# Optimization experiments

Measured on AMD Instinct MI355X. Metric: run time of the kernel, lower is better.

The kernel has to match this reference:

```python
import jax, jax.numpy as jnp
import numpy as np

B, N, DEG, LOOKBACK, DIM, OUT = 256, 512, 16, 5, 64, 6
E = B * N * DEG            # 2,097,152 directed edges
NN = B * N                 # 131,072 nodes
K1 = int(np.ceil(0.8 * N))    # 410 nodes kept per graph after pool1
K2 = int(np.ceil(0.8 * K1))   # 328 nodes kept per graph after pool2


def setup_inputs():
    key = jax.random.key(0)
    ks = jax.random.split(key, 14)
    x = jax.random.normal(ks[0], (NN, LOOKBACK), jnp.float32)
    # per-graph random edges, then shift into the global node index space
    local = jax.random.randint(ks[1], (2, E), 0, N)
    offsets = jnp.repeat(jnp.arange(B, dtype=jnp.int32) * N, N * DEG)
    edge_index = local + offsets[None, :]

    def lin(k, fi, fo):
        return jax.random.normal(k, (fi, fo), jnp.float32) / np.sqrt(fi)

    return {
        "x": x,
        "edge_index": edge_index,
        "c1_Wl": lin(ks[2], LOOKBACK, DIM), "c1_bl": jnp.zeros((DIM,), jnp.float32),
        "c1_Wr": lin(ks[3], LOOKBACK, DIM),
        "pool1_w": jax.random.normal(ks[4], (DIM,), jnp.float32) / np.sqrt(DIM),
        "c2_Wl": lin(ks[5], DIM, DIM), "c2_bl": jnp.zeros((DIM,), jnp.float32),
        "c2_Wr": lin(ks[6], DIM, DIM),
        "pool2_w": jax.random.normal(ks[7], (DIM,), jnp.float32) / np.sqrt(DIM),
        "lin1_W": lin(ks[8], 2 * DIM, DIM), "lin1_b": jnp.zeros((DIM,), jnp.float32),
        "lin2_W": lin(ks[9], DIM, OUT), "lin2_b": jnp.zeros((OUT,), jnp.float32),
    }


def _sage(x, src, dst, valid, Wl, bl, Wr, n_nodes):
    # PyG SAGEConv: out = lin_l(mean_{j->i} x_j) + lin_r(x_i); empty nbhd -> 0
    msg = x[src] * valid[:, None]
    s = jax.ops.segment_sum(msg, dst, num_segments=n_nodes)
    deg = jax.ops.segment_sum(valid, dst, num_segments=n_nodes)
    mean = s / jnp.maximum(deg, 1.0)[:, None]
    return mean @ Wl + bl + x @ Wr


def _topk(x, w, nb, npg, k):
    # PyG TopKPooling: score = tanh(x.w/||w||), keep top-k per graph, scale kept rows
    score = jnp.tanh((x @ w) / jnp.linalg.norm(w))
    vals, idx = jax.lax.top_k(score.reshape(nb, npg), k)     # [nb, k]
    perm = (idx + (jnp.arange(nb) * npg)[:, None]).reshape(-1)
    return x[perm] * vals.reshape(-1, 1), perm


def _readout(x, nb, k):
    r = x.reshape(nb, k, -1)
    return jnp.concatenate([r.max(axis=1), r.mean(axis=1)], axis=1)  # [gmp | gap]


def reference(x, edge_index, c1_Wl, c1_bl, c1_Wr, pool1_w,
              c2_Wl, c2_bl, c2_Wr, pool2_w, lin1_W, lin1_b, lin2_W, lin2_b):
    src, dst = edge_index[0], edge_index[1]
    valid0 = jnp.ones((E,), jnp.float32)

    h = jax.nn.relu(_sage(x, src, dst, valid0, c1_Wl, c1_bl, c1_Wr, NN))
    h, perm1 = _topk(h, pool1_w, B, N, K1)
    x1 = _readout(h, B, K1)

    # filter_adj: remap edges to pooled node ids, mask dropped edges
    n1 = B * K1
    inv = jnp.full((NN,), -1, jnp.int32).at[perm1].set(jnp.arange(n1, dtype=jnp.int32))
    s1, d1 = inv[src], inv[dst]
    valid1 = ((s1 >= 0) & (d1 >= 0)).astype(jnp.float32)
    s1 = jnp.maximum(s1, 0)
    d1 = jnp.maximum(d1, 0)

    h = jax.nn.relu(_sage(h, s1, d1, valid1, c2_Wl, c2_bl, c2_Wr, n1))
    h, _ = _topk(h, pool2_w, B, K1, K2)
    x2 = _readout(h, B, K2)

    z = x1 + x2
    z = jax.nn.relu(z @ lin1_W + lin1_b)
    return z @ lin2_W + lin2_b
```

## Files before the change

### kernel.cpp

```cpp
#include <hip/hip_runtime.h>
#include <hip/hip_bf16.h>

#define BGR   256
#define NPG1  512
#define DEG   16
#define EPG   (NPG1 * DEG)
#define LB    5
#define DIM   64
#define OUTF  6
#define NN    (BGR * NPG1)
#define EDG   (BGR * EPG)
#define K1    410
#define K2    328
#define N1    (BGR * K1)
#define K1P   (K1 + 1)
#define NR    (BGR * K1P)
#define CSRW  48
#define CSRW1 56
#define GRIDW (NR / 64)
#define GRIDA (N1 / 16)

__global__ __launch_bounds__(512)
void s1_csr_score_kernel(const float* __restrict__ x,
                         const int* __restrict__ eidx,
                         const float* __restrict__ Wl,
                         const float* __restrict__ bl,
                         const float* __restrict__ Wr,
                         const float* __restrict__ pw,
                         float* __restrict__ meanv,
                         float* __restrict__ sc1g) {
    __shared__ __align__(16) float xl[NPG1 * LB];
    __shared__ unsigned short lcsr[CSRW1 * NPG1];
    __shared__ int lcnt[NPG1];

    const int g = blockIdx.x, t = threadIdx.x;
    const int* __restrict__ src = eidx;
    const int* __restrict__ dst = eidx + EDG;

    {
        const float4* x4 = (const float4*)(x + (size_t)g * (NPG1 * LB));
        float4* xl4 = (float4*)xl;
        #pragma unroll
        for (int k = 0; k < 2; ++k) {
            int i = k * 512 + t;
            if (i < NPG1 * LB / 4) xl4[i] = x4[i];
        }
        lcnt[t] = 0;
    }
    __syncthreads();

    const int ebase = g * EPG;
    for (int k = 0; k < EPG / 512; ++k) {
        int e = ebase + k * 512 + t;
        int s = src[e] & (NPG1 - 1);
        int d = dst[e] & (NPG1 - 1);
        int slot = atomicAdd(&lcnt[d], 1);
        if (slot < CSRW1) lcsr[slot * NPG1 + d] = (unsigned short)s;
    }
    __syncthreads();

    const int dgf = lcnt[t];
    const int dg  = min(dgf, CSRW1);
    float s0 = 0.f, s1 = 0.f, s2 = 0.f, s3 = 0.f, s4 = 0.f;
    for (int k = 0; k < dg; ++k) {
        int s = lcsr[k * NPG1 + t];
        const float* xp = xl + s * LB;
        s0 += xp[0]; s1 += xp[1]; s2 += xp[2]; s3 += xp[3]; s4 += xp[4];
    }
    const float invd = 1.f / fmaxf((float)dgf, 1.f);
    float m[LB]  = { s0 * invd, s1 * invd, s2 * invd, s3 * invd, s4 * invd };
    float xv[LB];
    const int n = g * NPG1 + t;
    #pragma unroll
    for (int j = 0; j < LB; ++j) { xv[j] = xl[t * LB + j]; meanv[(size_t)n * LB + j] = m[j]; }

    const float4* Wl4 = (const float4*)Wl;
    const float4* Wr4 = (const float4*)Wr;
    const float4* bl4 = (const float4*)bl;
    const float4* pw4 = (const float4*)pw;
    float p = 0.f, q = 0.f;
    #pragma unroll 4
    for (int d4 = 0; d4 < DIM / 4; ++d4) {
        float4 bb = bl4[d4];
        float4 ww = pw4[d4];
        float4 h = bb;
        #pragma unroll
        for (int j = 0; j < LB; ++j) {
            float4 a = Wl4[j * (DIM / 4) + d4];
            float4 b = Wr4[j * (DIM / 4) + d4];
            h.x += m[j] * a.x + xv[j] * b.x;
            h.y += m[j] * a.y + xv[j] * b.y;
            h.z += m[j] * a.z + xv[j] * b.z;
            h.w += m[j] * a.w + xv[j] * b.w;
        }
        h.x = fmaxf(h.x, 0.f); h.y = fmaxf(h.y, 0.f);
        h.z = fmaxf(h.z, 0.f); h.w = fmaxf(h.w, 0.f);
        p += h.x * ww.x + h.y * ww.y + h.z * ww.z + h.w * ww.w;
        q += ww.x * ww.x + ww.y * ww.y + ww.z * ww.z + ww.w * ww.w;
    }
    sc1g[n] = tanhf(p / sqrtf(q));
}

__global__ __launch_bounds__(512)
void s1_rankpool_csr2_kernel(const float* __restrict__ x,
                             const float* __restrict__ meanv,
                             const float* __restrict__ sc1g,
                             const int* __restrict__ eidx,
                             const float* __restrict__ Wl,
                             const float* __restrict__ bl,
                             const float* __restrict__ Wr,
                             float* __restrict__ h1p,
                             float* __restrict__ x1buf,
                             unsigned short* __restrict__ csr2,
                             int* __restrict__ indeg) {
    __shared__ __align__(16) float sc[NPG1];
    __shared__ int   rnk[NPG1];
    __shared__ float redmx[8 * DIM];
    __shared__ float redsm[8 * DIM];
    __shared__ __align__(16) unsigned short lcsr2[K1 * CSRW];
    __shared__ int   lcnt2[K1];

    const int g = blockIdx.x, t = threadIdx.x;
    const int wid = t >> 6, lane = t & 63;
    const int* __restrict__ src = eidx;
    const int* __restrict__ dst = eidx + EDG;

    sc[t] = sc1g[g * NPG1 + t];
    if (t < DIM) h1p[((size_t)g * K1P + K1) * DIM + t] = 0.f;
    if (t < K1) lcnt2[t] = 0;
    {
        const int fill = (K1 << 16) | K1;
        int* li = (int*)lcsr2;
        for (int i = t; i < K1 * CSRW / 2; i += 512) li[i] = fill;
    }
    __syncthreads();

    {
        float my = sc[t];
        int r = 0;
        const float4* sc4 = (const float4*)sc;
        #pragma unroll 4
        for (int j4 = 0; j4 < NPG1 / 4; ++j4) {
            float4 v = sc4[j4];
            int j = 4 * j4;
            r += (v.x > my) | ((v.x == my) & (j     < t));
            r += (v.y > my) | ((v.y == my) & (j + 1 < t));
            r += (v.z > my) | ((v.z == my) & (j + 2 < t));
            r += (v.w > my) | ((v.w == my) & (j + 3 < t));
        }
        rnk[t] = r;
    }
    __syncthreads();

    const int ebase = g * EPG;
    for (int k = 0; k < EPG / 512; ++k) {
        int e = ebase + k * 512 + t;
        int rs = rnk[src[e] & (NPG1 - 1)];
        int rd = rnk[dst[e] & (NPG1 - 1)];
        if (rs < K1 && rd < K1) {
            int slot = atomicAdd(&lcnt2[rd], 1);
            if (slot < CSRW) lcsr2[rd * CSRW + slot] = (unsigned short)rs;
        }
    }

    float wlv[LB], wrv[LB];
    #pragma unroll
    for (int j = 0; j < LB; ++j) { wlv[j] = Wl[j * DIM + lane]; wrv[j] = Wr[j * DIM + lane]; }
    const float blv = bl[lane];

    float mx = -INFINITY, sm = 0.f;
    for (int n = wid; n < NPG1; n += 8) {
        int r = rnk[n];
        if (r >= K1) continue;
        const float* mp = meanv + (size_t)(g * NPG1 + n) * LB;
        const float* xp = x + (size_t)(g * NPG1 + n) * LB;
        float al = 0.f, ar = 0.f;
        #pragma unroll
        for (int j = 0; j < LB; ++j) {
            al += mp[j] * wlv[j];
            ar += xp[j] * wrv[j];
        }
        float acc = fmaxf(blv + al + ar, 0.f);
        float v = acc * sc[n];
        h1p[((size_t)g * K1P + r) * DIM + lane] = v;
        mx = fmaxf(mx, v);
        sm += v;
    }
    redmx[wid * DIM + lane] = mx;
    redsm[wid * DIM + lane] = sm;
    __syncthreads();

    if (wid == 0) {
        float m2 = redmx[lane], s2 = redsm[lane];
        #pragma unroll
        for (int w = 1; w < 8; ++w) {
            m2 = fmaxf(m2, redmx[w * DIM + lane]);
            s2 += redsm[w * DIM + lane];
        }
        x1buf[g * 2 * DIM + lane]       = m2;
        x1buf[g * 2 * DIM + DIM + lane] = s2 * (1.0f / (float)K1);
    }

    {
        const int4* ls4 = (const int4*)lcsr2;
        int4* gs4 = (int4*)(csr2 + (size_t)g * K1 * CSRW);
        for (int i = t; i < K1 * CSRW / 8; i += 512) gs4[i] = ls4[i];
        if (t < K1) indeg[g * K1 + t] = min(lcnt2[t], CSRW);
    }
}

__global__ __launch_bounds__(512)
void gemm2_kernel(float* __restrict__ hY,
                  float* __restrict__ Yr,
                  const float* __restrict__ Wl,
                  const float* __restrict__ bl,
                  const float* __restrict__ Wr) {
    __shared__ __align__(16) float wls[DIM * DIM];
    __shared__ __align__(16) float wrs[DIM * DIM];
    __shared__ __align__(16) float rt[64 * DIM];

    const int t = threadIdx.x, wid = t >> 6, lane = t & 63;
    const int nb = (int)blockIdx.x * 64;

    {
        const float4* W4l = (const float4*)Wl;
        const float4* W4r = (const float4*)Wr;
        const float4* R4  = (const float4*)&hY[(size_t)nb * DIM];
        float4* a = (float4*)wls;
        float4* b = (float4*)wrs;
        float4* r = (float4*)rt;
        #pragma unroll
        for (int k = 0; k < 2; ++k) {
            a[k * 512 + t] = W4l[k * 512 + t];
            b[k * 512 + t] = W4r[k * 512 + t];
            r[k * 512 + t] = R4[k * 512 + t];
        }
    }
    __syncthreads();

    const int r0 = wid * 8;
    float accl[8] = {0.f,0.f,0.f,0.f,0.f,0.f,0.f,0.f};
    float accr[8] = {0.f,0.f,0.f,0.f,0.f,0.f,0.f,0.f};
    #pragma unroll 4
    for (int j4 = 0; j4 < DIM / 4; ++j4) {
        const int jb = 4 * j4 * DIM + lane;
        float w0 = wls[jb],           w1 = wls[jb + DIM];
        float w2 = wls[jb + 2 * DIM], w3 = wls[jb + 3 * DIM];
        float u0 = wrs[jb],           u1 = wrs[jb + DIM];
        float u2 = wrs[jb + 2 * DIM], u3 = wrs[jb + 3 * DIM];
        #pragma unroll
        for (int i = 0; i < 8; ++i) {
            float4 a = *(const float4*)&rt[(r0 + i) * DIM + 4 * j4];
            accl[i] += a.x * w0 + a.y * w1 + a.z * w2 + a.w * w3;
            accr[i] += a.x * u0 + a.y * u1 + a.z * u2 + a.w * u3;
        }
    }
    const float bv = bl[lane];
    #pragma unroll
    for (int i = 0; i < 8; ++i) {
        hY[(size_t)(nb + r0 + i) * DIM + lane] = accl[i];
        Yr[(size_t)(nb + r0 + i) * DIM + lane] = accr[i] + bv;
    }
}

__global__ __launch_bounds__(256)
void gather2_kernel(const float* __restrict__ Yl,
                    float* __restrict__ Yh,
                    const unsigned short* __restrict__ csr2,
                    const int* __restrict__ indeg,
                    const float* __restrict__ pw,
                    float* __restrict__ sc2g) {
    const int t = threadIdx.x, wid = t >> 6, lane = t & 63;
    const int cid = ((int)blockIdx.x & 7) * (GRIDA / 8) + ((int)blockIdx.x >> 3);
    const int nb = __builtin_amdgcn_readfirstlane(cid * 16 + wid * 4);

    const float pwv = pw[lane];
    float q = pwv * pwv;
    #pragma unroll
    for (int o = 32; o; o >>= 1) q += __shfl_xor(q, o);
    const float inv_nrm = 1.f / sqrtf(q);

    #pragma unroll
    for (int i = 0; i < 4; ++i) {
        const int n  = nb + i;
        const int dg = indeg[n];
        const int g  = n / K1;
        const int lr = n - g * K1;
        const float* __restrict__ bp = Yl + (size_t)g * K1P * DIM;
        const int4* cr = (const int4*)(csr2 + (size_t)n * CSRW);
        float a0 = 0.f, a1 = 0.f;
        const int it = (dg + 7) >> 3;
        for (int kc = 0; kc < it; ++kc) {
            int4 wv = cr[kc];
            a0 += bp[((wv.x & 0xffff) << 6) + lane];
            a1 += bp[((wv.x >> 16)    << 6) + lane];
            a0 += bp[((wv.y & 0xffff) << 6) + lane];
            a1 += bp[((wv.y >> 16)    << 6) + lane];
            a0 += bp[((wv.z & 0xffff) << 6) + lane];
            a1 += bp[((wv.z >> 16)    << 6) + lane];
            a0 += bp[((wv.w & 0xffff) << 6) + lane];
            a1 += bp[((wv.w >> 16)    << 6) + lane];
        }
        const float invd = 1.f / fmaxf((float)dg, 1.f);
        float* yrow = Yh + (size_t)(g * K1P + lr) * DIM;
        const float h = fmaxf((a0 + a1) * invd + yrow[lane], 0.f);
        yrow[lane] = h;
        float p = h * pwv;
        #pragma unroll
        for (int o = 32; o; o >>= 1) p += __shfl_xor(p, o);
        if (lane == 0) sc2g[n] = tanhf(p * inv_nrm);
    }
}

__global__ __launch_bounds__(512)
void pool2_mlp_kernel(const float* __restrict__ sc2g,
                      const float* __restrict__ h2,
                      const float* __restrict__ x1buf,
                      const float* __restrict__ W1,
                      const float* __restrict__ b1,
                      const float* __restrict__ W2,
                      const float* __restrict__ b2,
                      float* __restrict__ out) {
    __shared__ __align__(16) float sc2[412];
    __shared__ int   rnk2[K1];
    __shared__ float redmx[8 * DIM];
    __shared__ float redsm[8 * DIM];
    __shared__ float zy[2 * DIM + DIM];

    const int g = blockIdx.x, t = threadIdx.x;
    const int wid = t >> 6, lane = t & 63;

    if (t < K1) sc2[t] = sc2g[g * K1 + t];
    if (t >= K1 && t < 412) sc2[t] = -INFINITY;
    __syncthreads();

    if (t < K1) {
        float my = sc2[t];
        int r = 0;
        const float4* sc4 = (const float4*)sc2;
        #pragma unroll 4
        for (int j4 = 0; j4 < 103; ++j4) {
            float4 v = sc4[j4];
            int j = 4 * j4;
            r += (v.x > my) | ((v.x == my) & (j     < t));
            r += (v.y > my) | ((v.y == my) & (j + 1 < t));
            r += (v.z > my) | ((v.z == my) & (j + 2 < t));
            r += (v.w > my) | ((v.w == my) & (j + 3 < t));
        }
        rnk2[t] = r;
    }
    __syncthreads();

    float mx = -INFINITY, sm = 0.f;
    for (int n = wid; n < K1; n += 8) {
        if (rnk2[n] < K2) {
            float v = h2[((size_t)g * K1P + n) * DIM + lane] * sc2[n];
            mx = fmaxf(mx, v);
            sm += v;
        }
    }
    redmx[wid * DIM + lane] = mx;
    redsm[wid * DIM + lane] = sm;
    __syncthreads();
    if (wid == 0) {
        float m2 = redmx[lane], s2 = redsm[lane];
        #pragma unroll
        for (int w = 1; w < 8; ++w) {
            m2 = fmaxf(m2, redmx[w * DIM + lane]);
            s2 += redsm[w * DIM + lane];
        }
        zy[lane]       = x1buf[g * 2 * DIM + lane]       + m2;
        zy[DIM + lane] = x1buf[g * 2 * DIM + DIM + lane] + s2 * (1.0f / (float)K2);
    }
    __syncthreads();

    if (t < DIM) {
        float a = b1[t];
        #pragma unroll 8
        for (int j = 0; j < 2 * DIM; ++j) a += zy[j] * W1[j * DIM + t];
        zy[2 * DIM + t] = fmaxf(a, 0.f);
    }
    __syncthreads();
    if (t < OUTF) {
        float a = b2[t];
        #pragma unroll
        for (int j = 0; j < DIM; ++j) a += zy[2 * DIM + j] * W2[j * OUTF + t];
        out[g * OUTF + t] = a;
    }
}

extern "C" void kernel_launch(void* const* d_in, const int* in_sizes, int n_in,
                              void* d_out, int out_size, void* d_ws, size_t ws_size,
                              hipStream_t stream) {
    (void)in_sizes; (void)n_in; (void)out_size; (void)ws_size;
    const float* x       = (const float*)d_in[0];
    const int*   eidx    = (const int*)d_in[1];
    const float* c1_Wl   = (const float*)d_in[2];
    const float* c1_bl   = (const float*)d_in[3];
    const float* c1_Wr   = (const float*)d_in[4];
    const float* pool1_w = (const float*)d_in[5];
    const float* c2_Wl   = (const float*)d_in[6];
    const float* c2_bl   = (const float*)d_in[7];
    const float* c2_Wr   = (const float*)d_in[8];
    const float* pool2_w = (const float*)d_in[9];
    const float* lin1_W  = (const float*)d_in[10];
    const float* lin1_b  = (const float*)d_in[11];
    const float* lin2_W  = (const float*)d_in[12];
    const float* lin2_b  = (const float*)d_in[13];
    float* out = (float*)d_out;

    char* w = (char*)d_ws;
    size_t off = 0;
    auto alloc = [&](size_t bytes) {
        void* p = w + off;
        off = (off + bytes + 255) & ~(size_t)255;
        return p;
    };
    float* h1p   = (float*)alloc((size_t)NR * DIM * 4);
    float* x1buf = (float*)alloc((size_t)BGR * 2 * DIM * 4);
    float* sc2g  = (float*)alloc((size_t)N1 * 4);
    int*   indeg = (int*)  alloc((size_t)N1 * 4);
    float* Yh    = (float*)alloc((size_t)NR * DIM * 4);
    unsigned short* csr2 = (unsigned short*)alloc((size_t)N1 * CSRW * 2);
    float* meanv = (float*)alloc((size_t)NN * LB * 4);
    float* sc1g  = (float*)alloc((size_t)NN * 4);

    float* Yl = h1p;

    s1_csr_score_kernel<<<BGR, 512, 0, stream>>>(x, eidx, c1_Wl, c1_bl, c1_Wr,
                                                 pool1_w, meanv, sc1g);
    s1_rankpool_csr2_kernel<<<BGR, 512, 0, stream>>>(x, meanv, sc1g, eidx,
                                                     c1_Wl, c1_bl, c1_Wr,
                                                     h1p, x1buf, csr2, indeg);
    gemm2_kernel<<<GRIDW, 512, 0, stream>>>(h1p, Yh, c2_Wl, c2_bl, c2_Wr);
    gather2_kernel<<<GRIDA, 256, 0, stream>>>(Yl, Yh, csr2, indeg, pool2_w, sc2g);
    pool2_mlp_kernel<<<BGR, 512, 0, stream>>>(sc2g, Yh, x1buf, lin1_W, lin1_b,
                                              lin2_W, lin2_b, out);
}
```

Baseline: 178.0 us.

## Fuse stage-1 CSR/score and rank-pool kernels, build pooled CSR from LDS CSR

Merges the two per-graph stage-1 kernels into one block so mean aggregates, scores and x stay in shared memory instead of round-tripping through global meanv/sc1g buffers. The pooled-graph CSR is now built per destination node by filtering the stage-1 LDS CSR through the rank table, which replaces a second pass over global edge indices and its shared-memory atomics. The cost is a much larger shared-memory footprint per block, which lowers occupancy. The CSR neighbor order also becomes deterministic per thread rather than set by atomic order.

New measurement: 165.8 us. -6.8%, faster.

```diff
diff --git a/kernel.cpp b/kernel.cpp
--- a/kernel.cpp
+++ b/kernel.cpp
@@ -21,19 +21,29 @@
 #define GRIDA (N1 / 16)
 
 __global__ __launch_bounds__(512)
-void s1_csr_score_kernel(const float* __restrict__ x,
-                         const int* __restrict__ eidx,
-                         const float* __restrict__ Wl,
-                         const float* __restrict__ bl,
-                         const float* __restrict__ Wr,
-                         const float* __restrict__ pw,
-                         float* __restrict__ meanv,
-                         float* __restrict__ sc1g) {
+void s1_mega_kernel(const float* __restrict__ x,
+                    const int* __restrict__ eidx,
+                    const float* __restrict__ Wl,
+                    const float* __restrict__ bl,
+                    const float* __restrict__ Wr,
+                    const float* __restrict__ pw,
+                    float* __restrict__ h1p,
+                    float* __restrict__ x1buf,
+                    unsigned short* __restrict__ csr2,
+                    int* __restrict__ indeg) {
     __shared__ __align__(16) float xl[NPG1 * LB];
-    __shared__ unsigned short lcsr[CSRW1 * NPG1];
-    __shared__ int lcnt[NPG1];
+    __shared__ __align__(16) float ml[NPG1 * LB];
+    __shared__ unsigned short lcsr1[CSRW1 * NPG1];
+    __shared__ int   lcnt[NPG1];
+    __shared__ __align__(16) float sc[NPG1];
+    __shared__ int   rnk[NPG1];
+    __shared__ __align__(16) unsigned short lcsr2[K1 * CSRW];
+    __shared__ int   lcnt2[K1];
+    __shared__ float redmx[8 * DIM];
+    __shared__ float redsm[8 * DIM];
 
     const int g = blockIdx.x, t = threadIdx.x;
+    const int wid = t >> 6, lane = t & 63;
     const int* __restrict__ src = eidx;
     const int* __restrict__ dst = eidx + EDG;
 
@@ -46,6 +56,10 @@
             if (i < NPG1 * LB / 4) xl4[i] = x4[i];
         }
         lcnt[t] = 0;
+        const int fill = (K1 << 16) | K1;
+        int* li = (int*)lcsr2;
+        for (int i = t; i < K1 * CSRW / 2; i += 512) li[i] = fill;
+        if (t < DIM) h1p[((size_t)g * K1P + K1) * DIM + t] = 0.f;
     }
     __syncthreads();
 
@@ -55,83 +69,50 @@
         int s = src[e] & (NPG1 - 1);
         int d = dst[e] & (NPG1 - 1);
         int slot = atomicAdd(&lcnt[d], 1);
-        if (slot < CSRW1) lcsr[slot * NPG1 + d] = (unsigned short)s;
-    }
-    __syncthreads();
-
-    const int dgf = lcnt[t];
-    const int dg  = min(dgf, CSRW1);
-    float s0 = 0.f, s1 = 0.f, s2 = 0.f, s3 = 0.f, s4 = 0.f;
-    for (int k = 0; k < dg; ++k) {
-        int s = lcsr[k * NPG1 + t];
-        const float* xp = xl + s * LB;
-        s0 += xp[0]; s1 += xp[1]; s2 += xp[2]; s3 += xp[3]; s4 += xp[4];
-    }
-    const float invd = 1.f / fmaxf((float)dgf, 1.f);
-    float m[LB]  = { s0 * invd, s1 * invd, s2 * invd, s3 * invd, s4 * invd };
-    float xv[LB];
-    const int n = g * NPG1 + t;
-    #pragma unroll
-    for (int j = 0; j < LB; ++j) { xv[j] = xl[t * LB + j]; meanv[(size_t)n * LB + j] = m[j]; }
-
-    const float4* Wl4 = (const float4*)Wl;
-    const float4* Wr4 = (const float4*)Wr;
-    const float4* bl4 = (const float4*)bl;
-    const float4* pw4 = (const float4*)pw;
-    float p = 0.f, q = 0.f;
-    #pragma unroll 4
-    for (int d4 = 0; d4 < DIM / 4; ++d4) {
-        float4 bb = bl4[d4];
-        float4 ww = pw4[d4];
-        float4 h = bb;
-        #pragma unroll
-        for (int j = 0; j < LB; ++j) {
-            float4 a = Wl4[j * (DIM / 4) + d4];
-            float4 b = Wr4[j * (DIM / 4) + d4];
-            h.x += m[j] * a.x + xv[j] * b.x;
-            h.y += m[j] * a.y + xv[j] * b.y;
-            h.z += m[j] * a.z + xv[j] * b.z;
-            h.w += m[j] * a.w + xv[j] * b.w;
-        }
-        h.x = fmaxf(h.x, 0.f); h.y = fmaxf(h.y, 0.f);
-        h.z = fmaxf(h.z, 0.f); h.w = fmaxf(h.w, 0.f);
-        p += h.x * ww.x + h.y * ww.y + h.z * ww.z + h.w * ww.w;
-        q += ww.x * ww.x + ww.y * ww.y + ww.z * ww.z + ww.w * ww.w;
-    }
-    sc1g[n] = tanhf(p / sqrtf(q));
-}
-
-__global__ __launch_bounds__(512)
-void s1_rankpool_csr2_kernel(const float* __restrict__ x,
-                             const float* __restrict__ meanv,
-                             const float* __restrict__ sc1g,
-                             const int* __restrict__ eidx,
-                             const float* __restrict__ Wl,
-                             const float* __restrict__ bl,
-                             const float* __restrict__ Wr,
-                             float* __restrict__ h1p,
-                             float* __restrict__ x1buf,
-                             unsigned short* __restrict__ csr2,
-                             int* __restrict__ indeg) {
-    __shared__ __align__(16) float sc[NPG1];
-    __shared__ int   rnk[NPG1];
-    __shared__ float redmx[8 * DIM];
-    __shared__ float redsm[8 * DIM];
-    __shared__ __align__(16) unsigned short lcsr2[K1 * CSRW];
-    __shared__ int   lcnt2[K1];
-
-    const int g = blockIdx.x, t = threadIdx.x;
-    const int wid = t >> 6, lane = t & 63;
-    const int* __restrict__ src = eidx;
-    const int* __restrict__ dst = eidx + EDG;
-
-    sc[t] = sc1g[g * NPG1 + t];
-    if (t < DIM) h1p[((size_t)g * K1P + K1) * DIM + t] = 0.f;
-    if (t < K1) lcnt2[t] = 0;
-    {
-        const int fill = (K1 << 16) | K1;
-        int* li = (int*)lcsr2;
-        for (int i = t; i < K1 * CSRW / 2; i += 512) li[i] = fill;
+        if (slot < CSRW1) lcsr1[slot * NPG1 + d] = (unsigned short)s;
+    }
+    __syncthreads();
+
+    {
+        const int dgf = lcnt[t];
+        const int dg  = min(dgf, CSRW1);
+        float s0 = 0.f, s1 = 0.f, s2 = 0.f, s3 = 0.f, s4 = 0.f;
+        for (int k = 0; k < dg; ++k) {
+            int s = lcsr1[k * NPG1 + t];
+            const float* xp = xl + s * LB;
+            s0 += xp[0]; s1 += xp[1]; s2 += xp[2]; s3 += xp[3]; s4 += xp[4];
+        }
+        const float invd = 1.f / fmaxf((float)dgf, 1.f);
+        float m[LB]  = { s0 * invd, s1 * invd, s2 * invd, s3 * invd, s4 * invd };
+        float xv[LB];
+        #pragma unroll
+        for (int j = 0; j < LB; ++j) { xv[j] = xl[t * LB + j]; ml[t * LB + j] = m[j]; }
+
+        const float4* Wl4 = (const float4*)Wl;
+        const float4* Wr4 = (const float4*)Wr;
+        const float4* bl4 = (const float4*)bl;
+        const float4* pw4 = (const float4*)pw;
+        float p = 0.f, q = 0.f;
+        #pragma unroll 4
+        for (int d4 = 0; d4 < DIM / 4; ++d4) {
+            float4 bb = bl4[d4];
+            float4 ww = pw4[d4];
+            float4 h = bb;
+            #pragma unroll
+            for (int j = 0; j < LB; ++j) {
+                float4 a = Wl4[j * (DIM / 4) + d4];
+                float4 b = Wr4[j * (DIM / 4) + d4];
+                h.x += m[j] * a.x + xv[j] * b.x;
+                h.y += m[j] * a.y + xv[j] * b.y;
+                h.z += m[j] * a.z + xv[j] * b.z;
+                h.w += m[j] * a.w + xv[j] * b.w;
+            }
+            h.x = fmaxf(h.x, 0.f); h.y = fmaxf(h.y, 0.f);
+            h.z = fmaxf(h.z, 0.f); h.w = fmaxf(h.w, 0.f);
+            p += h.x * ww.x + h.y * ww.y + h.z * ww.z + h.w * ww.w;
+            q += ww.x * ww.x + ww.y * ww.y + ww.z * ww.z + ww.w * ww.w;
+        }
+        sc[t] = tanhf(p / sqrtf(q));
     }
     __syncthreads();
 
@@ -152,42 +133,50 @@
     }
     __syncthreads();
 
-    const int ebase = g * EPG;
-    for (int k = 0; k < EPG / 512; ++k) {
-        int e = ebase + k * 512 + t;
-        int rs = rnk[src[e] & (NPG1 - 1)];
-        int rd = rnk[dst[e] & (NPG1 - 1)];
-        if (rs < K1 && rd < K1) {
-            int slot = atomicAdd(&lcnt2[rd], 1);
-            if (slot < CSRW) lcsr2[rd * CSRW + slot] = (unsigned short)rs;
-        }
-    }
-
-    float wlv[LB], wrv[LB];
-    #pragma unroll
-    for (int j = 0; j < LB; ++j) { wlv[j] = Wl[j * DIM + lane]; wrv[j] = Wr[j * DIM + lane]; }
-    const float blv = bl[lane];
-
-    float mx = -INFINITY, sm = 0.f;
-    for (int n = wid; n < NPG1; n += 8) {
-        int r = rnk[n];
-        if (r >= K1) continue;
-        const float* mp = meanv + (size_t)(g * NPG1 + n) * LB;
-        const float* xp = x + (size_t)(g * NPG1 + n) * LB;
-        float al = 0.f, ar = 0.f;
-        #pragma unroll
-        for (int j = 0; j < LB; ++j) {
-            al += mp[j] * wlv[j];
-            ar += xp[j] * wrv[j];
-        }
-        float acc = fmaxf(blv + al + ar, 0.f);
-        float v = acc * sc[n];
-        h1p[((size_t)g * K1P + r) * DIM + lane] = v;
-        mx = fmaxf(mx, v);
-        sm += v;
-    }
-    redmx[wid * DIM + lane] = mx;
-    redsm[wid * DIM + lane] = sm;
+    {
+        const int rd = rnk[t];
+        if (rd < K1) {
+            const int dg1 = min(lcnt[t], CSRW1);
+            int vcnt = 0;
+            for (int k = 0; k < dg1; ++k) {
+                int s  = lcsr1[k * NPG1 + t];
+                int rs = rnk[s];
+                if (rs < K1) {
+                    if (vcnt < CSRW) lcsr2[rd * CSRW + vcnt] = (unsigned short)rs;
+                    ++vcnt;
+                }
+            }
+            lcnt2[rd] = min(vcnt, CSRW);
+        }
+    }
+
+    {
+        float wlv[LB], wrv[LB];
+        #pragma unroll
+        for (int j = 0; j < LB; ++j) { wlv[j] = Wl[j * DIM + lane]; wrv[j] = Wr[j * DIM + lane]; }
+        const float blv = bl[lane];
+
+        float mx = -INFINITY, sm = 0.f;
+        for (int n = wid; n < NPG1; n += 8) {
+            int r = rnk[n];
+            if (r >= K1) continue;
+            const float* mp = ml + n * LB;
+            const float* xp = xl + n * LB;
+            float al = 0.f, ar = 0.f;
+            #pragma unroll
+            for (int j = 0; j < LB; ++j) {
+                al += mp[j] * wlv[j];
+                ar += xp[j] * wrv[j];
+            }
+            float acc = fmaxf(blv + al + ar, 0.f);
+            float v = acc * sc[n];
+            h1p[((size_t)g * K1P + r) * DIM + lane] = v;
+            mx = fmaxf(mx, v);
+            sm += v;
+        }
+        redmx[wid * DIM + lane] = mx;
+        redsm[wid * DIM + lane] = sm;
+    }
     __syncthreads();
 
     if (wid == 0) {
@@ -205,7 +194,7 @@
         const int4* ls4 = (const int4*)lcsr2;
         int4* gs4 = (int4*)(csr2 + (size_t)g * K1 * CSRW);
         for (int i = t; i < K1 * CSRW / 8; i += 512) gs4[i] = ls4[i];
-        if (t < K1) indeg[g * K1 + t] = min(lcnt2[t], CSRW);
+        if (t < K1) indeg[g * K1 + t] = lcnt2[t];
     }
 }
 
@@ -422,16 +411,11 @@
     int*   indeg = (int*)  alloc((size_t)N1 * 4);
     float* Yh    = (float*)alloc((size_t)NR * DIM * 4);
     unsigned short* csr2 = (unsigned short*)alloc((size_t)N1 * CSRW * 2);
-    float* meanv = (float*)alloc((size_t)NN * LB * 4);
-    float* sc1g  = (float*)alloc((size_t)NN * 4);
 
     float* Yl = h1p;
 
-    s1_csr_score_kernel<<<BGR, 512, 0, stream>>>(x, eidx, c1_Wl, c1_bl, c1_Wr,
-                                                 pool1_w, meanv, sc1g);
-    s1_rankpool_csr2_kernel<<<BGR, 512, 0, stream>>>(x, meanv, sc1g, eidx,
-                                                     c1_Wl, c1_bl, c1_Wr,
-                                                     h1p, x1buf, csr2, indeg);
+    s1_mega_kernel<<<BGR, 512, 0, stream>>>(x, eidx, c1_Wl, c1_bl, c1_Wr,
+                                            pool1_w, h1p, x1buf, csr2, indeg);
     gemm2_kernel<<<GRIDW, 512, 0, stream>>>(h1p, Yh, c2_Wl, c2_bl, c2_Wr);
     gather2_kernel<<<GRIDA, 256, 0, stream>>>(Yl, Yh, csr2, indeg, pool2_w, sc2g);
     pool2_mlp_kernel<<<BGR, 512, 0, stream>>>(sc2g, Yh, x1buf, lin1_W, lin1_b,
```
